# Kernel tuning notes

Hardware: AMD Instinct MI355X
Metric: run time of the kernel (lower is better)

## Reference

```python
import jax, jax.numpy as jnp
import numpy as np

VOCAB = 32000
HID = 2048
MAXLEN = 128


def setup_inputs() -> dict:
    key = jax.random.key(0)
    ks = jax.random.split(key, 16)
    s = 0.02
    return {
        "input_seq": jax.random.randint(ks[0], (1, 1), 0, VOCAB),
        "hidden": jax.random.normal(ks[1], (1, 1, HID), jnp.float32),
        "encoder_outputs": jax.random.normal(ks[2], (MAXLEN, HID), jnp.float32),
        "emb": jax.random.normal(ks[3], (VOCAB, HID), jnp.float32) * s,
        "attn_W": jax.random.normal(ks[4], (MAXLEN, 2 * HID), jnp.float32) * s,
        "attn_b": jnp.zeros((MAXLEN,), jnp.float32),
        "comb_W": jax.random.normal(ks[5], (HID, 2 * HID), jnp.float32) * s,
        "comb_b": jnp.zeros((HID,), jnp.float32),
        "W_ih": jax.random.normal(ks[6], (HID, HID), jnp.float32) * s,
        "W_hh": jax.random.normal(ks[7], (HID, HID), jnp.float32) * s,
        "b_ih": jnp.zeros((HID,), jnp.float32),
        "b_hh": jnp.zeros((HID,), jnp.float32),
        "out_W": jax.random.normal(ks[8], (VOCAB, HID), jnp.float32) * s,
        "out_b": jnp.zeros((VOCAB,), jnp.float32),
    }


def _rnn_step(x, h, W_ih, W_hh, b_ih, b_hh):
    # Elman RNN cell (tanh): seq_len=1 so output == new hidden. Shapes [1,1,H].
    return jnp.tanh(x @ W_ih.T + b_ih + h @ W_hh.T + b_hh)


def reference(input_seq, hidden, encoder_outputs, emb, attn_W, attn_b,
              comb_W, comb_b, W_ih, W_hh, b_ih, b_hh, out_W, out_b):
    tok = input_seq[0]                       # [1]
    x = emb[tok].reshape(1, 1, -1)           # [1,1,H]
    hidden = _rnn_step(x, hidden, W_ih, W_hh, b_ih, b_hh)   # [1,1,H]
    # second embedding of the decoder token (dropout is identity at eval)
    embedded = emb[tok].reshape(1, 1, -1)    # [1,1,H]
    attn_in = jnp.concatenate([embedded[0], hidden[0]], axis=1)   # [1,2H]
    attn_weights = jax.nn.softmax(attn_in @ attn_W.T + attn_b, axis=1)  # [1,L]
    attn_applied = attn_weights @ encoder_outputs                 # [1,H]
    o = jnp.concatenate([embedded[0], attn_applied], axis=1) @ comb_W.T + comb_b
    o = jax.nn.relu(o)[None]                 # [1,1,H]
    out_h = _rnn_step(o, hidden, W_ih, W_hh, b_ih, b_hh)          # [1,1,H]
    logits = out_h[0] @ out_W.T + out_b      # [1,VOCAB]
    return jax.nn.log_softmax(logits, axis=1)
```

## Files before the change

kernel.cpp:

```cpp
#include <hip/hip_runtime.h>
#include <math.h>

#define HID 2048
#define MAXLEN 128
#define VOCAB 32000

__device__ __forceinline__ float wave_sum(float v) {
    #pragma unroll
    for (int m = 1; m < 64; m <<= 1) v += __shfl_xor(v, m, 64);
    return v;
}

__device__ __forceinline__ float dot4(float4 a, float4 b) {
    return a.x * b.x + a.y * b.y + a.z * b.z + a.w * b.w;
}

__device__ __forceinline__ float block_sum256(float v) {
    __shared__ float s[4];
    v = wave_sum(v);
    const int lane = threadIdx.x & 63, w = threadIdx.x >> 6;
    if (lane == 0) s[w] = v;
    __syncthreads();
    return s[0] + s[1] + s[2] + s[3];
}

__device__ __forceinline__ float row_dot2048(const float4* __restrict__ w,
                                             const float4* __restrict__ x) {
    const int t = threadIdx.x;
    return dot4(w[t], x[t]) + dot4(w[t + 256], x[t + 256]);
}

__global__ __launch_bounds__(256)
void k1_fused_left(const float* __restrict__ W_ih, const float* __restrict__ W_hh,
                   const float* __restrict__ emb, const int* __restrict__ tok,
                   const float* __restrict__ hidden,
                   const float* __restrict__ b_ih, const float* __restrict__ b_hh,
                   const float* __restrict__ attn_W, const float* __restrict__ attn_b,
                   const float* __restrict__ comb_W, const float* __restrict__ comb_b,
                   float* __restrict__ H1, float* __restrict__ ALe,
                   float* __restrict__ Oe) {
    const float4* xemb = (const float4*)(emb + (size_t)tok[0] * HID);
    const int bid = blockIdx.x, t = threadIdx.x;
    if (bid < HID) {
        const float4* w1 = (const float4*)(W_ih + (size_t)bid * HID);
        const float4* w2 = (const float4*)(W_hh + (size_t)bid * HID);
        float p = row_dot2048(w1, xemb) + row_dot2048(w2, (const float4*)hidden);
        p = block_sum256(p);
        if (t == 0) H1[bid] = tanhf(p + b_ih[bid] + b_hh[bid]);
    } else if (bid < HID + MAXLEN) {
        const int l = bid - HID;
        const float4* w = (const float4*)(attn_W + (size_t)l * 2 * HID);
        float p = block_sum256(row_dot2048(w, xemb));
        if (t == 0) ALe[l] = p + attn_b[l];
    } else {
        const int r = bid - HID - MAXLEN;
        const float4* w = (const float4*)(comb_W + (size_t)r * 2 * HID);
        float p = block_sum256(row_dot2048(w, xemb));
        if (t == 0) Oe[r] = p + comb_b[r];
    }
}

__global__ __launch_bounds__(256)
void k2_attn_right(const float* __restrict__ attn_W, const float* __restrict__ H1,
                   const float* __restrict__ ALe, float* __restrict__ AL) {
    const int l = blockIdx.x, t = threadIdx.x;
    const float4* w = (const float4*)(attn_W + (size_t)l * 2 * HID + HID);
    float p = block_sum256(row_dot2048(w, (const float4*)H1));
    if (t == 0) AL[l] = ALe[l] + p;
}

__global__ __launch_bounds__(256)
void k3_softmax_apply(const float* __restrict__ AL, const float* __restrict__ enc,
                      float* __restrict__ AA) {
    __shared__ float sAL[MAXLEN];
    __shared__ float wts[MAXLEN];
    __shared__ float cs[4][64];
    const int t = threadIdx.x;
    if (t < MAXLEN) sAL[t] = AL[t];
    __syncthreads();
    float m = sAL[0];
    for (int l = 1; l < MAXLEN; ++l) m = fmaxf(m, sAL[l]);
    float s = 0.f;
    for (int l = 0; l < MAXLEN; ++l) s += expf(sAL[l] - m);
    if (t < MAXLEN) wts[t] = expf(sAL[t] - m) / s;
    __syncthreads();
    const int j  = blockIdx.x * 64 + (t & 63);
    const int l0 = t >> 6;
    float acc = 0.f;
    #pragma unroll 8
    for (int l = l0; l < MAXLEN; l += 4) acc += wts[l] * enc[(size_t)l * HID + j];
    cs[l0][t & 63] = acc;
    __syncthreads();
    if (t < 64) AA[blockIdx.x * 64 + t] = cs[0][t] + cs[1][t] + cs[2][t] + cs[3][t];
}

__global__ __launch_bounds__(256)
void k4_comb_right(const float* __restrict__ comb_W, const float* __restrict__ AA,
                   const float* __restrict__ Oe, float* __restrict__ O) {
    const int r = blockIdx.x, t = threadIdx.x;
    const float4* w = (const float4*)(comb_W + (size_t)r * 2 * HID + HID);
    float p = block_sum256(row_dot2048(w, (const float4*)AA));
    if (t == 0) O[r] = fmaxf(Oe[r] + p, 0.f);
}

__global__ __launch_bounds__(256)
void k5_rnn2(const float* __restrict__ W_ih, const float* __restrict__ W_hh,
             const float* __restrict__ O, const float* __restrict__ H1,
             const float* __restrict__ b_ih, const float* __restrict__ b_hh,
             float* __restrict__ OH) {
    const int r = blockIdx.x, t = threadIdx.x;
    const float4* w1 = (const float4*)(W_ih + (size_t)r * HID);
    const float4* w2 = (const float4*)(W_hh + (size_t)r * HID);
    float p = row_dot2048(w1, (const float4*)O) + row_dot2048(w2, (const float4*)H1);
    p = block_sum256(p);
    if (t == 0) OH[r] = tanhf(p + b_ih[r] + b_hh[r]);
}

__global__ __launch_bounds__(256)
void k6_bigmv(const float* __restrict__ W, const float* __restrict__ x,
              const float* __restrict__ b, float* __restrict__ out,
              float* __restrict__ PE) {
    __shared__ float red[4];
    const int wid = threadIdx.x >> 6, lane = threadIdx.x & 63;
    const int r0 = blockIdx.x * 8 + wid * 2;
    const float4* xv = (const float4*)x;
    const float4* w0 = (const float4*)(W + (size_t)r0 * HID);
    const float4* w1 = (const float4*)(W + (size_t)(r0 + 1) * HID);
    float a0 = 0.f, a1 = 0.f;
    #pragma unroll
    for (int k = 0; k < 8; ++k) {
        const float4 xc = xv[lane + k * 64];
        a0 += dot4(w0[lane + k * 64], xc);
        a1 += dot4(w1[lane + k * 64], xc);
    }
    a0 = wave_sum(a0);
    a1 = wave_sum(a1);
    if (lane == 0) {
        a0 += b[r0];
        a1 += b[r0 + 1];
        out[r0] = a0;
        out[r0 + 1] = a1;
        red[wid] = expf(a0) + expf(a1);
    }
    __syncthreads();
    if (threadIdx.x == 0) PE[blockIdx.x] = red[0] + red[1] + red[2] + red[3];
}

__global__ __launch_bounds__(256)
void k7_lse_apply(const float* __restrict__ PE, float* __restrict__ out) {
    const int t = threadIdx.x;
    float s = 0.f;
    for (int i = t; i < VOCAB / 8; i += 256) s += PE[i];
    const float lg = logf(block_sum256(s));
    out[blockIdx.x * 256 + t] -= lg;
}

extern "C" void kernel_launch(void* const* d_in, const int* in_sizes, int n_in,
                              void* d_out, int out_size, void* d_ws, size_t ws_size,
                              hipStream_t stream) {
    const int*   tok    = (const int*)  d_in[0];
    const float* hidden = (const float*)d_in[1];
    const float* enc    = (const float*)d_in[2];
    const float* emb    = (const float*)d_in[3];
    const float* attn_W = (const float*)d_in[4];
    const float* attn_b = (const float*)d_in[5];
    const float* comb_W = (const float*)d_in[6];
    const float* comb_b = (const float*)d_in[7];
    const float* W_ih   = (const float*)d_in[8];
    const float* W_hh   = (const float*)d_in[9];
    const float* b_ih   = (const float*)d_in[10];
    const float* b_hh   = (const float*)d_in[11];
    const float* out_W  = (const float*)d_in[12];
    const float* out_b  = (const float*)d_in[13];
    float* out = (float*)d_out;

    float* ws  = (float*)d_ws;
    float* H1  = ws;
    float* ALe = ws + 2048;
    float* AL  = ws + 2176;
    float* AA  = ws + 2304;
    float* Oe  = ws + 4352;
    float* O   = ws + 6400;
    float* OH  = ws + 8448;
    float* PE  = ws + 10496;

    k1_fused_left<<<HID + MAXLEN + HID, 256, 0, stream>>>(W_ih, W_hh, emb, tok, hidden,
                                                          b_ih, b_hh, attn_W, attn_b,
                                                          comb_W, comb_b, H1, ALe, Oe);
    k2_attn_right<<<MAXLEN, 256, 0, stream>>>(attn_W, H1, ALe, AL);
    k3_softmax_apply<<<HID / 64, 256, 0, stream>>>(AL, enc, AA);
    k4_comb_right<<<HID, 256, 0, stream>>>(comb_W, AA, Oe, O);
    k5_rnn2<<<HID, 256, 0, stream>>>(W_ih, W_hh, O, H1, b_ih, b_hh, OH);
    k6_bigmv<<<VOCAB / 8, 256, 0, stream>>>(out_W, OH, out_b, out, PE);
    k7_lse_apply<<<VOCAB / 256, 256, 0, stream>>>(PE, out);
}
```

Measured before the change: 85.97 us.

## Fuse attention logits into softmax-apply kernel and widen vocab GEMV rows

Merges the attention right-half matvec into the softmax/apply kernel. Each of the 32 blocks recomputes all 128 attention logits redundantly, which removes one launch and the AL round trip through global memory. The output projection now processes 4 rows per wave with nontemporal loads and vectorized bias/output stores, halving the block count. The cost is that the attention logits are recomputed 32 times, about 1 MB of attn_W reads each time, mostly served from L2.

```diff
diff --git a/kernel.cpp b/kernel.cpp
--- a/kernel.cpp
+++ b/kernel.cpp
@@ -4,6 +4,8 @@
 #define HID 2048
 #define MAXLEN 128
 #define VOCAB 32000
+
+typedef float f4 __attribute__((ext_vector_type(4)));
 
 __device__ __forceinline__ float wave_sum(float v) {
     #pragma unroll
@@ -13,6 +15,12 @@
 
 __device__ __forceinline__ float dot4(float4 a, float4 b) {
     return a.x * b.x + a.y * b.y + a.z * b.z + a.w * b.w;
+}
+__device__ __forceinline__ float dot4v(f4 a, f4 b) {
+    return a.x * b.x + a.y * b.y + a.z * b.z + a.w * b.w;
+}
+__device__ __forceinline__ f4 ntload(const f4* p) {
+    return __builtin_nontemporal_load(p);
 }
 
 __device__ __forceinline__ float block_sum256(float v) {
@@ -61,22 +69,23 @@
 }
 
 __global__ __launch_bounds__(256)
-void k2_attn_right(const float* __restrict__ attn_W, const float* __restrict__ H1,
-                   const float* __restrict__ ALe, float* __restrict__ AL) {
-    const int l = blockIdx.x, t = threadIdx.x;
-    const float4* w = (const float4*)(attn_W + (size_t)l * 2 * HID + HID);
-    float p = block_sum256(row_dot2048(w, (const float4*)H1));
-    if (t == 0) AL[l] = ALe[l] + p;
-}
-
-__global__ __launch_bounds__(256)
-void k3_softmax_apply(const float* __restrict__ AL, const float* __restrict__ enc,
-                      float* __restrict__ AA) {
+void k23_attn_softmax_apply(const float* __restrict__ attn_W,
+                            const float* __restrict__ H1, const float* __restrict__ ALe,
+                            const float* __restrict__ enc, float* __restrict__ AA) {
     __shared__ float sAL[MAXLEN];
     __shared__ float wts[MAXLEN];
     __shared__ float cs[4][64];
-    const int t = threadIdx.x;
-    if (t < MAXLEN) sAL[t] = AL[t];
+    const int t = threadIdx.x, lane = t & 63, wid = t >> 6;
+    const float4* h1 = (const float4*)H1;
+    for (int li = 0; li < 32; ++li) {
+        const int l = wid * 32 + li;
+        const float4* w = (const float4*)(attn_W + (size_t)l * 2 * HID + HID);
+        float p = 0.f;
+        #pragma unroll
+        for (int k = 0; k < 8; ++k) p += dot4(w[lane + k * 64], h1[lane + k * 64]);
+        p = wave_sum(p);
+        if (lane == 0) sAL[l] = ALe[l] + p;
+    }
     __syncthreads();
     float m = sAL[0];
     for (int l = 1; l < MAXLEN; ++l) m = fmaxf(m, sAL[l]);
@@ -84,12 +93,11 @@
     for (int l = 0; l < MAXLEN; ++l) s += expf(sAL[l] - m);
     if (t < MAXLEN) wts[t] = expf(sAL[t] - m) / s;
     __syncthreads();
-    const int j  = blockIdx.x * 64 + (t & 63);
-    const int l0 = t >> 6;
+    const int j = blockIdx.x * 64 + lane;
     float acc = 0.f;
     #pragma unroll 8
-    for (int l = l0; l < MAXLEN; l += 4) acc += wts[l] * enc[(size_t)l * HID + j];
-    cs[l0][t & 63] = acc;
+    for (int l = wid; l < MAXLEN; l += 4) acc += wts[l] * enc[(size_t)l * HID + j];
+    cs[wid][lane] = acc;
     __syncthreads();
     if (t < 64) AA[blockIdx.x * 64 + t] = cs[0][t] + cs[1][t] + cs[2][t] + cs[3][t];
 }
@@ -122,25 +130,32 @@
               float* __restrict__ PE) {
     __shared__ float red[4];
     const int wid = threadIdx.x >> 6, lane = threadIdx.x & 63;
-    const int r0 = blockIdx.x * 8 + wid * 2;
-    const float4* xv = (const float4*)x;
-    const float4* w0 = (const float4*)(W + (size_t)r0 * HID);
-    const float4* w1 = (const float4*)(W + (size_t)(r0 + 1) * HID);
-    float a0 = 0.f, a1 = 0.f;
+    const int r0 = blockIdx.x * 16 + wid * 4;
+    const f4* xv = (const f4*)x;
+    const f4* w0 = (const f4*)(W + (size_t)r0 * HID);
+    const f4* w1 = w0 + 512;
+    const f4* w2 = w0 + 1024;
+    const f4* w3 = w0 + 1536;
+    float a0 = 0.f, a1 = 0.f, a2 = 0.f, a3 = 0.f;
     #pragma unroll
     for (int k = 0; k < 8; ++k) {
-        const float4 xc = xv[lane + k * 64];
-        a0 += dot4(w0[lane + k * 64], xc);
-        a1 += dot4(w1[lane + k * 64], xc);
+        const int idx = lane + k * 64;
+        const f4 xc = xv[idx];
+        a0 += dot4v(ntload(w0 + idx), xc);
+        a1 += dot4v(ntload(w1 + idx), xc);
+        a2 += dot4v(ntload(w2 + idx), xc);
+        a3 += dot4v(ntload(w3 + idx), xc);
     }
     a0 = wave_sum(a0);
     a1 = wave_sum(a1);
+    a2 = wave_sum(a2);
+    a3 = wave_sum(a3);
     if (lane == 0) {
-        a0 += b[r0];
-        a1 += b[r0 + 1];
-        out[r0] = a0;
-        out[r0 + 1] = a1;
-        red[wid] = expf(a0) + expf(a1);
+        const f4 bb = *(const f4*)(b + r0);
+        a0 += bb.x; a1 += bb.y; a2 += bb.z; a3 += bb.w;
+        f4 o; o.x = a0; o.y = a1; o.z = a2; o.w = a3;
+        *(f4*)(out + r0) = o;
+        red[wid] = expf(a0) + expf(a1) + expf(a2) + expf(a3);
     }
     __syncthreads();
     if (threadIdx.x == 0) PE[blockIdx.x] = red[0] + red[1] + red[2] + red[3];
@@ -150,7 +165,7 @@
 void k7_lse_apply(const float* __restrict__ PE, float* __restrict__ out) {
     const int t = threadIdx.x;
     float s = 0.f;
-    for (int i = t; i < VOCAB / 8; i += 256) s += PE[i];
+    for (int i = t; i < VOCAB / 16; i += 256) s += PE[i];
     const float lg = logf(block_sum256(s));
     out[blockIdx.x * 256 + t] -= lg;
 }
@@ -177,7 +192,6 @@
     float* ws  = (float*)d_ws;
     float* H1  = ws;
     float* ALe = ws + 2048;
-    float* AL  = ws + 2176;
     float* AA  = ws + 2304;
     float* Oe  = ws + 4352;
     float* O   = ws + 6400;
@@ -187,10 +201,9 @@
     k1_fused_left<<<HID + MAXLEN + HID, 256, 0, stream>>>(W_ih, W_hh, emb, tok, hidden,
                                                           b_ih, b_hh, attn_W, attn_b,
                                                           comb_W, comb_b, H1, ALe, Oe);
-    k2_attn_right<<<MAXLEN, 256, 0, stream>>>(attn_W, H1, ALe, AL);
-    k3_softmax_apply<<<HID / 64, 256, 0, stream>>>(AL, enc, AA);
+    k23_attn_softmax_apply<<<HID / 64, 256, 0, stream>>>(attn_W, H1, ALe, enc, AA);
     k4_comb_right<<<HID, 256, 0, stream>>>(comb_W, AA, Oe, O);
     k5_rnn2<<<HID, 256, 0, stream>>>(W_ih, W_hh, O, H1, b_ih, b_hh, OH);
-    k6_bigmv<<<VOCAB / 8, 256, 0, stream>>>(out_W, OH, out_b, out, PE);
+    k6_bigmv<<<VOCAB / 16, 256, 0, stream>>>(out_W, OH, out_b, out, PE);
     k7_lse_apply<<<VOCAB / 256, 256, 0, stream>>>(PE, out);
 }
```

Measured after the change: 156.6 us. +82.2%, slower.
